# Kernel tuning notes

Measured on AMD Instinct MI355X. Metric: run time of the kernel, lower is better.

## Reference

```python
import jax, jax.numpy as jnp
import numpy as np

V = 50000
E = 800000
B, FIN, FOUT, K = 2, 64, 64, 4


def setup_inputs() -> dict:
    key = jax.random.key(0)
    k1, k2, k3, k4, k5, k6 = jax.random.split(key, 6)
    inputs = jax.random.normal(k1, (B, V, FIN), dtype=jnp.float32)
    weight = jax.random.normal(k2, (K, FIN, FOUT), dtype=jnp.float32) * np.sqrt(2.0 / (FIN * K)).astype(np.float32)
    bias = jax.random.normal(k3, (FOUT,), dtype=jnp.float32)
    lap_vals = jax.random.normal(k4, (E,), dtype=jnp.float32)
    lap_rows = jax.random.randint(k5, (E,), 0, V, dtype=jnp.int32)
    lap_cols = jax.random.randint(k6, (E,), 0, V, dtype=jnp.int32)
    return {"inputs": inputs, "weight": weight, "bias": bias,
            "lap_vals": lap_vals, "lap_rows": lap_rows, "lap_cols": lap_cols}


def reference(inputs, weight, bias, lap_vals, lap_rows, lap_cols):
    B_, V_, Fin = inputs.shape
    K_, _, Fout = weight.shape

    def spmm(x):  # L @ x, L in COO; x: [V, Fin*B]
        return jax.ops.segment_sum(lap_vals[:, None] * x[lap_cols], lap_rows, num_segments=V_)

    # x0: [V, Fin*B] (Fin-major flatten, matching torch permute(1,2,0).view)
    x0 = jnp.transpose(inputs, (1, 2, 0)).reshape(V_, Fin * B_)
    xs = [x0]
    if K_ > 1:
        x1 = spmm(x0)
        xs.append(x1)
        for _ in range(2, K_):
            x2 = 2.0 * spmm(x1) - x0
            xs.append(x2)
            x0, x1 = x1, x2
    # [K,V,Fin,B] -> [B,V,Fin,K] -> [B*V, Fin*K]
    X = jnp.stack(xs).reshape(K_, V_, Fin, B_)
    X = jnp.transpose(X, (3, 1, 2, 0)).reshape(B_ * V_, Fin * K_)
    # faithful to original: weight flattened as (K*Fin, Fout)
    out = X @ weight.reshape(K_ * Fin, Fout)
    return out.reshape(B_, V_, Fout) + bias
```

## Files before the change

kernel.cpp:

```cpp
#include <hip/hip_runtime.h>
#include <hip/hip_bf16.h>


#define NV 50000
#define NE 800000
#define XROW 128
#define NROWS 100000
#define NTILES 6250
#define EPMAX 1600000
#define BSHIFT 7
#define RPB 128
#define NB 391
#define CAP 3072
#define CHUNK 4096
#define P1_BLOCKS 196

using u16 = unsigned short;
using u32 = unsigned int;
using u64 = unsigned long long;
typedef __bf16 bf16x8 __attribute__((ext_vector_type(8)));
typedef float f32x4 __attribute__((ext_vector_type(4)));

__device__ __forceinline__ float bflo(u32 g) { return __uint_as_float(g << 16); }
__device__ __forceinline__ float bfhi(u32 g) { return __uint_as_float(g & 0xffff0000u); }
__device__ __forceinline__ u32 pack_bf2(float a, float b) {
    u16 ha = __builtin_bit_cast(u16, (__bf16)a);
    u16 hb = __builtin_bit_cast(u16, (__bf16)b);
    return (u32)ha | ((u32)hb << 16);
}
__device__ __forceinline__ float unpack_f16hi(u32 rec) {
    u16 h = (u16)(rec >> 16);
    return (float)__builtin_bit_cast(_Float16, h);
}
__device__ __forceinline__ int pad16(int n) { return (n + 15) & ~15; }

__global__ __launch_bounds__(256) void bin1_k(const int* __restrict__ rows, const int* __restrict__ cols,
                                              const float* __restrict__ vals,
                                              int* __restrict__ binctr, u64* __restrict__ tmp) {
    __shared__ int bcnt[NB];
    __shared__ int bofs[NB];
    __shared__ int bcur[NB];
    __shared__ int gbase[NB];
    __shared__ int ps[256];
    __shared__ u64 stage[CHUNK];
    int t = threadIdx.x;
    int base = blockIdx.x * CHUNK;
    int n = NE - base;
    if (n > CHUNK) n = CHUNK;
    if (n <= 0) return;

    for (int i = t; i < NB; i += 256) bcnt[i] = 0;
    __syncthreads();

    for (int i = t; i < n; i += 256) {
        atomicAdd(&bcnt[rows[base + i] >> BSHIFT], 1);
    }
    __syncthreads();

    int i0 = 2 * t, i1 = 2 * t + 1;
    int a0 = (i0 < NB) ? bcnt[i0] : 0;
    int a1 = (i1 < NB) ? bcnt[i1] : 0;
    ps[t] = a0 + a1;
    __syncthreads();
    for (int off = 1; off < 256; off <<= 1) {
        int v = (t >= off) ? ps[t - off] : 0;
        __syncthreads();
        ps[t] += v;
        __syncthreads();
    }
    int eb = ps[t] - (a0 + a1);
    if (i0 < NB) { bofs[i0] = eb;      bcur[i0] = eb;      gbase[i0] = i0 * CAP + atomicAdd(&binctr[i0], a0); }
    if (i1 < NB) { bofs[i1] = eb + a0; bcur[i1] = eb + a0; gbase[i1] = i1 * CAP + atomicAdd(&binctr[i1], a1); }
    __syncthreads();

    for (int i = t; i < n; i += 256) {
        int r = rows[base + i];
        int c = cols[base + i];
        u16 hv = __builtin_bit_cast(u16, (_Float16)vals[base + i]);
        u64 rec = ((u64)(u32)r << 32) | (u64)((u32)c | ((u32)hv << 16));
        int s = atomicAdd(&bcur[r >> BSHIFT], 1);
        stage[s] = rec;
    }
    __syncthreads();

    for (int i = t; i < n; i += 256) {
        u64 rec = stage[i];
        int b = (int)(rec >> (32 + BSHIFT));
        tmp[(size_t)(gbase[b] + (i - bofs[b]))] = rec;
    }
}

__global__ __launch_bounds__(256) void bcnt_k(const u64* __restrict__ tmp, const int* __restrict__ binctr,
                                              int* __restrict__ rowc, int* __restrict__ btot) {
    __shared__ int rc[RPB];
    __shared__ int rs[RPB];
    int b = blockIdx.x, t = threadIdx.x;
    int n = binctr[b];
    const u64* rec = tmp + (size_t)b * CAP;
    if (t < RPB) rc[t] = 0;
    __syncthreads();
    for (int i = t; i < n; i += 256) {
        atomicAdd(&rc[(int)(rec[i] >> 32) & (RPB - 1)], 1);
    }
    __syncthreads();
    if (t < RPB) {
        rowc[b * RPB + t] = rc[t];
        rs[t] = pad16(rc[t]);
    }
    __syncthreads();
    for (int off = 64; off > 0; off >>= 1) {
        if (t < off) rs[t] += rs[t + off];
        __syncthreads();
    }
    if (t == 0) btot[b] = rs[0];
}

__global__ __launch_bounds__(256) void scanb_k(const int* __restrict__ btot, int* __restrict__ bbase,
                                               int* __restrict__ row_ptr) {
    __shared__ int ps[256];
    int t = threadIdx.x;
    int i0 = 2 * t, i1 = 2 * t + 1;
    int a0 = (i0 < NB) ? btot[i0] : 0;
    int a1 = (i1 < NB) ? btot[i1] : 0;
    ps[t] = a0 + a1;
    __syncthreads();
    for (int off = 1; off < 256; off <<= 1) {
        int v = (t >= off) ? ps[t - off] : 0;
        __syncthreads();
        ps[t] += v;
        __syncthreads();
    }
    int eb = ps[t] - (a0 + a1);
    if (i0 < NB) bbase[i0] = eb;
    if (i1 < NB) bbase[i1] = eb + a0;
    if (t == 255) row_ptr[NV] = ps[255];
}

__global__ __launch_bounds__(256) void place_k(const u64* __restrict__ tmp, const int* __restrict__ binctr,
                                               const int* __restrict__ rowc, const int* __restrict__ bbase,
                                               int* __restrict__ row_ptr, u32* __restrict__ epack) {
    __shared__ int rc[RPB];
    __shared__ int ro[RPB];
    int b = blockIdx.x, t = threadIdx.x;
    int n = binctr[b];
    int base = bbase[b];
    const u64* rec = tmp + (size_t)b * CAP;

    int cv = (t < RPB) ? rowc[b * RPB + t] : 0;
    int pv = pad16(cv);
    if (t < RPB) ro[t] = pv;
    __syncthreads();
    for (int off = 1; off < RPB; off <<= 1) {
        int v = 0;
        if (t < RPB && t >= off) v = ro[t - off];
        __syncthreads();
        if (t < RPB) ro[t] += v;
        __syncthreads();
    }
    if (t < RPB) {
        int ex = ro[t] - pv;
        ro[t] = ex;
        rc[t] = 0;
        int v = (b << BSHIFT) + t;
        if (v < NV) row_ptr[v] = base + ex;
    }
    __syncthreads();
    for (int i = t; i < n; i += 256) {
        u64 r64 = rec[i];
        int r = (int)(r64 >> 32) & (RPB - 1);
        int p = base + ro[r] + atomicAdd(&rc[r], 1);
        epack[p] = (u32)r64;
    }
}

__global__ void build_x0_k(const float* __restrict__ in, u32* __restrict__ x0u) {
    int i = blockIdx.x * blockDim.x + threadIdx.x;
    if (i < NV * 64) {
        int v = i >> 6, p = i & 63;
        int b = p >> 5;
        int f = (p & 31) * 2;
        const float* src = in + (size_t)b * (NV * 64) + (size_t)v * 64 + f;
        float2 t = *(const float2*)src;
        x0u[i] = pack_bf2(t.x, t.y);
    }
}

__global__ void prep_w_k(const float* __restrict__ weight, u16* __restrict__ wimg) {
    int i = blockIdx.x * blockDim.x + threadIdx.x;
    if (i < 256 * 64) {
        int c = i >> 6, o = i & 63;
        int cp = ((c & 3) << 6) | (c >> 2);
        wimg[o * 264 + cp] = __builtin_bit_cast(u16, (__bf16)weight[i]);
    }
}

__global__ __launch_bounds__(256) void spmm_k(const u32* __restrict__ x,
                                              const u32* __restrict__ xprev,
                                              const int* __restrict__ row_ptr,
                                              const u32* __restrict__ epack,
                                              u32* __restrict__ xout, int mode) {
    int wave = (int)((blockIdx.x * blockDim.x + threadIdx.x) >> 6);
    u32 lane = threadIdx.x & 63;
    int row = __builtin_amdgcn_readfirstlane(wave);
    if (row >= NV) return;
    int beg = row_ptr[row];
    int end = row_ptr[row + 1];
    int q = (int)(lane >> 4);
    u32 g16 = lane & 15;

    float ax[4] = {0.f, 0.f, 0.f, 0.f};
    float ay[4] = {0.f, 0.f, 0.f, 0.f};

    for (int e = beg; e < end; e += 16) {
        u32 rec[4];
        uint4 gv[4];
        #pragma unroll
        for (int u = 0; u < 4; ++u) {
            rec[u] = epack[e + 4 * u + q];
            gv[u] = *(const uint4*)(x + ((rec[u] & 0xffffu) << 6) + (g16 << 2));
        }
        #pragma unroll
        for (int u = 0; u < 4; ++u) {
            float w = unpack_f16hi(rec[u]);
            ax[0] += w * bflo(gv[u].x); ay[0] += w * bfhi(gv[u].x);
            ax[1] += w * bflo(gv[u].y); ay[1] += w * bfhi(gv[u].y);
            ax[2] += w * bflo(gv[u].z); ay[2] += w * bfhi(gv[u].z);
            ax[3] += w * bflo(gv[u].w); ay[3] += w * bfhi(gv[u].w);
        }
    }

    #pragma unroll
    for (int m = 16; m <= 32; m <<= 1) {
        #pragma unroll
        for (int j = 0; j < 4; ++j) {
            ax[j] += __shfl_xor(ax[j], m, 64);
            ay[j] += __shfl_xor(ay[j], m, 64);
        }
    }

    if (q == 0) {
        if (mode) {
            uint4 pv = *(const uint4*)(xprev + ((u32)row << 6) + (g16 << 2));
            ax[0] = 2.f * ax[0] - bflo(pv.x); ay[0] = 2.f * ay[0] - bfhi(pv.x);
            ax[1] = 2.f * ax[1] - bflo(pv.y); ay[1] = 2.f * ay[1] - bfhi(pv.y);
            ax[2] = 2.f * ax[2] - bflo(pv.z); ay[2] = 2.f * ay[2] - bfhi(pv.z);
            ax[3] = 2.f * ax[3] - bflo(pv.w); ay[3] = 2.f * ay[3] - bfhi(pv.w);
        }
        uint4 o;
        o.x = pack_bf2(ax[0], ay[0]);
        o.y = pack_bf2(ax[1], ay[1]);
        o.z = pack_bf2(ax[2], ay[2]);
        o.w = pack_bf2(ax[3], ay[3]);
        *(uint4*)(xout + ((u32)row << 6) + (g16 << 2)) = o;
    }
}

__global__ __launch_bounds__(256) void final_k(const u16* __restrict__ x_all,
                                               const u16* __restrict__ wimg,
                                               const float* __restrict__ bias,
                                               float* __restrict__ out) {
    __shared__ u16 Wt[64 * 264];
    {
        const u32* src = (const u32*)wimg;
        u32* dst = (u32*)Wt;
        #pragma unroll 4
        for (int i = threadIdx.x; i < 64 * 264 / 2; i += 256) dst[i] = src[i];
    }
    __syncthreads();

    int lane = threadIdx.x & 63;
    int wid = threadIdx.x >> 6;
    int pair = blockIdx.x * 4 + wid;
    int t0 = pair * 2;
    if (t0 >= NTILES) return;

    int m = lane & 15;
    int q8 = (lane >> 4) * 8;

    int r0 = t0 * 16 + m;
    int r1 = r0 + 16;
    const u16* arow0 = x_all + (size_t)(r0 >> 1) * XROW + (r0 & 1) * 64;
    const u16* arow1 = x_all + (size_t)(r1 >> 1) * XROW + (r1 & 1) * 64;

    f32x4 accA[4] = {{0,0,0,0},{0,0,0,0},{0,0,0,0},{0,0,0,0}};
    f32x4 accB[4] = {{0,0,0,0},{0,0,0,0},{0,0,0,0},{0,0,0,0}};

    #pragma unroll
    for (int kb = 0; kb < 8; ++kb) {
        int cb = kb * 32 + q8;
        int arr = cb >> 6;
        int f0 = cb & 63;
        size_t aoff = (size_t)arr * (NV * XROW) + f0;
        bf16x8 a0 = *(const bf16x8*)(arow0 + aoff);
        bf16x8 a1 = *(const bf16x8*)(arow1 + aoff);
        #pragma unroll
        for (int j = 0; j < 4; ++j) {
            bf16x8 bj = *(const bf16x8*)&Wt[(j * 16 + m) * 264 + kb * 32 + q8];
            accA[j] = __builtin_amdgcn_mfma_f32_16x16x32_bf16(a0, bj, accA[j], 0, 0, 0);
            accB[j] = __builtin_amdgcn_mfma_f32_16x16x32_bf16(a1, bj, accB[j], 0, 0, 0);
        }
    }

    float bv[4];
    #pragma unroll
    for (int j = 0; j < 4; ++j) bv[j] = bias[j * 16 + m];

    #pragma unroll
    for (int half = 0; half < 2; ++half) {
        int rbase = (t0 + half) * 16 + (lane >> 4) * 4;
        f32x4* acc = half ? accB : accA;
        #pragma unroll
        for (int reg = 0; reg < 4; ++reg) {
            int rr = rbase + reg;
            float* op = out + (size_t)(rr & 1) * (NV * 64) + (size_t)(rr >> 1) * 64;
            #pragma unroll
            for (int j = 0; j < 4; ++j) op[j * 16 + m] = acc[j][reg] + bv[j];
        }
    }
}

extern "C" void kernel_launch(void* const* d_in, const int* in_sizes, int n_in,
                              void* d_out, int out_size, void* d_ws, size_t ws_size,
                              hipStream_t stream) {
    const float* inputs = (const float*)d_in[0];
    const float* weight = (const float*)d_in[1];
    const float* bias   = (const float*)d_in[2];
    const float* lapv   = (const float*)d_in[3];
    const int*   lrows  = (const int*)d_in[4];
    const int*   lcols  = (const int*)d_in[5];
    float* out = (float*)d_out;

    char* ws = (char*)d_ws;
    size_t o = 0;
    auto alloc = [&](size_t bytes) -> void* {
        void* p = ws + o;
        o += (bytes + 255) & ~(size_t)255;
        return p;
    };
    u16* x_all = (u16*)alloc((size_t)4 * NV * XROW * 2);
    u32* epack = (u32*)alloc((size_t)EPMAX * 4);
    u64* tmp   = (u64*)alloc((size_t)NB * CAP * 8);
    int* row_ptr = (int*)alloc((size_t)(NV + 1) * 4);
    int* binctr  = (int*)alloc((size_t)NB * 4);
    int* btot    = (int*)alloc((size_t)NB * 4);
    int* bbase   = (int*)alloc((size_t)NB * 4);
    int* rowc    = (int*)alloc((size_t)NB * RPB * 4);
    u16* wimg = (u16*)alloc((size_t)64 * 264 * 2);
    (void)ws_size; (void)in_sizes; (void)n_in; (void)out_size;

    u32* x0 = (u32*)(x_all + (size_t)0 * NV * XROW);
    u32* x1 = (u32*)(x_all + (size_t)1 * NV * XROW);
    u32* x2 = (u32*)(x_all + (size_t)2 * NV * XROW);
    u32* x3 = (u32*)(x_all + (size_t)3 * NV * XROW);

    hipMemsetAsync(binctr, 0, (size_t)NB * 4, stream);
    hipMemsetAsync(epack, 0, (size_t)EPMAX * 4, stream);
    bin1_k<<<P1_BLOCKS, 256, 0, stream>>>(lrows, lcols, lapv, binctr, tmp);
    bcnt_k<<<NB, 256, 0, stream>>>(tmp, binctr, rowc, btot);
    scanb_k<<<1, 256, 0, stream>>>(btot, bbase, row_ptr);
    place_k<<<NB, 256, 0, stream>>>(tmp, binctr, rowc, bbase, row_ptr, epack);
    build_x0_k<<<(NV * 64 + 255) / 256, 256, 0, stream>>>(inputs, x0);
    prep_w_k<<<64, 256, 0, stream>>>(weight, wimg);

    spmm_k<<<(NV + 3) / 4, 256, 0, stream>>>(x0, nullptr, row_ptr, epack, x1, 0);
    spmm_k<<<(NV + 3) / 4, 256, 0, stream>>>(x1, x0, row_ptr, epack, x2, 1);
    spmm_k<<<(NV + 3) / 4, 256, 0, stream>>>(x2, x1, row_ptr, epack, x3, 1);

    final_k<<<(NTILES / 2 + 3) / 4, 256, 0, stream>>>(x_all, wimg, bias, out);
}
```

Before: 230.9 us.

## Process two rows per wave in SpMM and zero only padding slots

Each SpMM wave now handles two adjacent rows, interleaving their edge-record and gather loads so more independent memory requests are in flight per wave. The grid shrinks by half. The full memset of the edge array is replaced by zeroing only the padded tail slots of each row inside the placement kernel. This raises register use and adds branch divergence when the two rows have different lengths.

Measured after the change: 239.9 us. +3.9%, slower.

```diff
diff --git a/kernel.cpp b/kernel.cpp
--- a/kernel.cpp
+++ b/kernel.cpp
@@ -14,6 +14,7 @@
 #define CAP 3072
 #define CHUNK 4096
 #define P1_BLOCKS 196
+#define NPAIR 25000
 
 using u16 = unsigned short;
 using u32 = unsigned int;
@@ -171,6 +172,12 @@
         int p = base + ro[r] + atomicAdd(&rc[r], 1);
         epack[p] = (u32)r64;
     }
+    __syncthreads();
+    if (t < RPB) {
+        int s = base + ro[t] + cv;
+        int e = base + ro[t] + pv;
+        for (int i = s; i < e; ++i) epack[i] = 0;
+    }
 }
 
 __global__ void build_x0_k(const float* __restrict__ in, u32* __restrict__ x0u) {
@@ -201,56 +208,95 @@
                                               u32* __restrict__ xout, int mode) {
     int wave = (int)((blockIdx.x * blockDim.x + threadIdx.x) >> 6);
     u32 lane = threadIdx.x & 63;
-    int row = __builtin_amdgcn_readfirstlane(wave);
-    if (row >= NV) return;
-    int beg = row_ptr[row];
-    int end = row_ptr[row + 1];
+    int row0 = __builtin_amdgcn_readfirstlane(wave) * 2;
+    if (row0 >= NV) return;
     int q = (int)(lane >> 4);
     u32 g16 = lane & 15;
 
-    float ax[4] = {0.f, 0.f, 0.f, 0.f};
-    float ay[4] = {0.f, 0.f, 0.f, 0.f};
-
-    for (int e = beg; e < end; e += 16) {
-        u32 rec[4];
-        uint4 gv[4];
-        #pragma unroll
-        for (int u = 0; u < 4; ++u) {
-            rec[u] = epack[e + 4 * u + q];
-            gv[u] = *(const uint4*)(x + ((rec[u] & 0xffffu) << 6) + (g16 << 2));
-        }
-        #pragma unroll
-        for (int u = 0; u < 4; ++u) {
-            float w = unpack_f16hi(rec[u]);
-            ax[0] += w * bflo(gv[u].x); ay[0] += w * bfhi(gv[u].x);
-            ax[1] += w * bflo(gv[u].y); ay[1] += w * bfhi(gv[u].y);
-            ax[2] += w * bflo(gv[u].z); ay[2] += w * bfhi(gv[u].z);
-            ax[3] += w * bflo(gv[u].w); ay[3] += w * bfhi(gv[u].w);
-        }
+    int beg0 = row_ptr[row0];
+    int mid  = row_ptr[row0 + 1];
+    int end1 = row_ptr[row0 + 2];
+
+    float ax0[4] = {0.f,0.f,0.f,0.f}, ay0[4] = {0.f,0.f,0.f,0.f};
+    float ax1[4] = {0.f,0.f,0.f,0.f}, ay1[4] = {0.f,0.f,0.f,0.f};
+
+    int e0 = beg0, e1 = mid;
+    while (e0 < mid || e1 < end1) {
+        bool a0 = e0 < mid, a1 = e1 < end1;
+        u32 rec0[4], rec1[4];
+        uint4 gv0[4], gv1[4];
+        if (a0) {
+            #pragma unroll
+            for (int u = 0; u < 4; ++u) rec0[u] = epack[e0 + 4 * u + q];
+        }
+        if (a1) {
+            #pragma unroll
+            for (int u = 0; u < 4; ++u) rec1[u] = epack[e1 + 4 * u + q];
+        }
+        if (a0) {
+            #pragma unroll
+            for (int u = 0; u < 4; ++u)
+                gv0[u] = *(const uint4*)(x + ((rec0[u] & 0xffffu) << 6) + (g16 << 2));
+        }
+        if (a1) {
+            #pragma unroll
+            for (int u = 0; u < 4; ++u)
+                gv1[u] = *(const uint4*)(x + ((rec1[u] & 0xffffu) << 6) + (g16 << 2));
+        }
+        if (a0) {
+            #pragma unroll
+            for (int u = 0; u < 4; ++u) {
+                float w = unpack_f16hi(rec0[u]);
+                ax0[0] += w * bflo(gv0[u].x); ay0[0] += w * bfhi(gv0[u].x);
+                ax0[1] += w * bflo(gv0[u].y); ay0[1] += w * bfhi(gv0[u].y);
+                ax0[2] += w * bflo(gv0[u].z); ay0[2] += w * bfhi(gv0[u].z);
+                ax0[3] += w * bflo(gv0[u].w); ay0[3] += w * bfhi(gv0[u].w);
+            }
+        }
+        if (a1) {
+            #pragma unroll
+            for (int u = 0; u < 4; ++u) {
+                float w = unpack_f16hi(rec1[u]);
+                ax1[0] += w * bflo(gv1[u].x); ay1[0] += w * bfhi(gv1[u].x);
+                ax1[1] += w * bflo(gv1[u].y); ay1[1] += w * bfhi(gv1[u].y);
+                ax1[2] += w * bflo(gv1[u].z); ay1[2] += w * bfhi(gv1[u].z);
+                ax1[3] += w * bflo(gv1[u].w); ay1[3] += w * bfhi(gv1[u].w);
+            }
+        }
+        e0 += 16; e1 += 16;
     }
 
     #pragma unroll
     for (int m = 16; m <= 32; m <<= 1) {
         #pragma unroll
         for (int j = 0; j < 4; ++j) {
-            ax[j] += __shfl_xor(ax[j], m, 64);
-            ay[j] += __shfl_xor(ay[j], m, 64);
-        }
-    }
-
-    if (q == 0) {
+            ax0[j] += __shfl_xor(ax0[j], m, 64);
+            ay0[j] += __shfl_xor(ay0[j], m, 64);
+            ax1[j] += __shfl_xor(ax1[j], m, 64);
+            ay1[j] += __shfl_xor(ay1[j], m, 64);
+        }
+    }
+
+    if (q < 2) {
+        int row = row0 + q;
+        float bx[4], by[4];
+        #pragma unroll
+        for (int j = 0; j < 4; ++j) {
+            bx[j] = q ? ax1[j] : ax0[j];
+            by[j] = q ? ay1[j] : ay0[j];
+        }
         if (mode) {
             uint4 pv = *(const uint4*)(xprev + ((u32)row << 6) + (g16 << 2));
-            ax[0] = 2.f * ax[0] - bflo(pv.x); ay[0] = 2.f * ay[0] - bfhi(pv.x);
-            ax[1] = 2.f * ax[1] - bflo(pv.y); ay[1] = 2.f * ay[1] - bfhi(pv.y);
-            ax[2] = 2.f * ax[2] - bflo(pv.z); ay[2] = 2.f * ay[2] - bfhi(pv.z);
-            ax[3] = 2.f * ax[3] - bflo(pv.w); ay[3] = 2.f * ay[3] - bfhi(pv.w);
+            bx[0] = 2.f * bx[0] - bflo(pv.x); by[0] = 2.f * by[0] - bfhi(pv.x);
+            bx[1] = 2.f * bx[1] - bflo(pv.y); by[1] = 2.f * by[1] - bfhi(pv.y);
+            bx[2] = 2.f * bx[2] - bflo(pv.z); by[2] = 2.f * by[2] - bfhi(pv.z);
+            bx[3] = 2.f * bx[3] - bflo(pv.w); by[3] = 2.f * by[3] - bfhi(pv.w);
         }
         uint4 o;
-        o.x = pack_bf2(ax[0], ay[0]);
-        o.y = pack_bf2(ax[1], ay[1]);
-        o.z = pack_bf2(ax[2], ay[2]);
-        o.w = pack_bf2(ax[3], ay[3]);
+        o.x = pack_bf2(bx[0], by[0]);
+        o.y = pack_bf2(bx[1], by[1]);
+        o.z = pack_bf2(bx[2], by[2]);
+        o.w = pack_bf2(bx[3], by[3]);
         *(uint4*)(xout + ((u32)row << 6) + (g16 << 2)) = o;
     }
 }
@@ -354,7 +400,6 @@
     u32* x3 = (u32*)(x_all + (size_t)3 * NV * XROW);
 
     hipMemsetAsync(binctr, 0, (size_t)NB * 4, stream);
-    hipMemsetAsync(epack, 0, (size_t)EPMAX * 4, stream);
     bin1_k<<<P1_BLOCKS, 256, 0, stream>>>(lrows, lcols, lapv, binctr, tmp);
     bcnt_k<<<NB, 256, 0, stream>>>(tmp, binctr, rowc, btot);
     scanb_k<<<1, 256, 0, stream>>>(btot, bbase, row_ptr);
@@ -362,9 +407,9 @@
     build_x0_k<<<(NV * 64 + 255) / 256, 256, 0, stream>>>(inputs, x0);
     prep_w_k<<<64, 256, 0, stream>>>(weight, wimg);
 
-    spmm_k<<<(NV + 3) / 4, 256, 0, stream>>>(x0, nullptr, row_ptr, epack, x1, 0);
-    spmm_k<<<(NV + 3) / 4, 256, 0, stream>>>(x1, x0, row_ptr, epack, x2, 1);
-    spmm_k<<<(NV + 3) / 4, 256, 0, stream>>>(x2, x1, row_ptr, epack, x3, 1);
+    spmm_k<<<(NPAIR + 3) / 4, 256, 0, stream>>>(x0, nullptr, row_ptr, epack, x1, 0);
+    spmm_k<<<(NPAIR + 3) / 4, 256, 0, stream>>>(x1, x0, row_ptr, epack, x2, 1);
+    spmm_k<<<(NPAIR + 3) / 4, 256, 0, stream>>>(x2, x1, row_ptr, epack, x3, 1);
 
     final_k<<<(NTILES / 2 + 3) / 4, 256, 0, stream>>>(x_all, wimg, bias, out);
 }
```

## Fuse scan into count kernel, merge prep kernels, pad rows to 32, unroll SpMM 8x

Applied to the files above, without the earlier changes.

Merges the single-block bin scan into the count kernel using a last-block-done atomic ticket, and combines the x0 build and weight prep into one launch. This removes several kernel launches and the large epack memset, which is replaced by zeroing only the padding slots in place_k. Row padding goes from 16 to 32 and the SpMM loop now issues 8 gathers per iteration for more memory-level parallelism. The cost is more padding work on short rows and a threadfence/atomic handshake between blocks.

New measurement: 234.8 us. About the same (+1.7%).

```diff
diff --git a/kernel.cpp b/kernel.cpp
--- a/kernel.cpp
+++ b/kernel.cpp
@@ -7,13 +7,14 @@
 #define XROW 128
 #define NROWS 100000
 #define NTILES 6250
-#define EPMAX 1600000
+#define EPMAX 1700000
 #define BSHIFT 7
 #define RPB 128
 #define NB 391
 #define CAP 3072
 #define CHUNK 4096
 #define P1_BLOCKS 196
+#define X0_BLOCKS 12500
 
 using u16 = unsigned short;
 using u32 = unsigned int;
@@ -32,7 +33,7 @@
     u16 h = (u16)(rec >> 16);
     return (float)__builtin_bit_cast(_Float16, h);
 }
-__device__ __forceinline__ int pad16(int n) { return (n + 15) & ~15; }
+__device__ __forceinline__ int pad32(int n) { return (n + 31) & ~31; }
 
 __global__ __launch_bounds__(256) void bin1_k(const int* __restrict__ rows, const int* __restrict__ cols,
                                               const float* __restrict__ vals,
@@ -91,9 +92,13 @@
 }
 
 __global__ __launch_bounds__(256) void bcnt_k(const u64* __restrict__ tmp, const int* __restrict__ binctr,
-                                              int* __restrict__ rowc, int* __restrict__ btot) {
+                                              int* __restrict__ rowc, int* __restrict__ btot,
+                                              int* __restrict__ done,
+                                              int* __restrict__ bbase, int* __restrict__ row_ptr) {
     __shared__ int rc[RPB];
     __shared__ int rs[RPB];
+    __shared__ int ps[256];
+    __shared__ int flag;
     int b = blockIdx.x, t = threadIdx.x;
     int n = binctr[b];
     const u64* rec = tmp + (size_t)b * CAP;
@@ -105,35 +110,38 @@
     __syncthreads();
     if (t < RPB) {
         rowc[b * RPB + t] = rc[t];
-        rs[t] = pad16(rc[t]);
+        rs[t] = pad32(rc[t]);
     }
     __syncthreads();
     for (int off = 64; off > 0; off >>= 1) {
         if (t < off) rs[t] += rs[t + off];
         __syncthreads();
     }
-    if (t == 0) btot[b] = rs[0];
-}
-
-__global__ __launch_bounds__(256) void scanb_k(const int* __restrict__ btot, int* __restrict__ bbase,
-                                               int* __restrict__ row_ptr) {
-    __shared__ int ps[256];
-    int t = threadIdx.x;
-    int i0 = 2 * t, i1 = 2 * t + 1;
-    int a0 = (i0 < NB) ? btot[i0] : 0;
-    int a1 = (i1 < NB) ? btot[i1] : 0;
-    ps[t] = a0 + a1;
-    __syncthreads();
-    for (int off = 1; off < 256; off <<= 1) {
-        int v = (t >= off) ? ps[t - off] : 0;
-        __syncthreads();
-        ps[t] += v;
-        __syncthreads();
-    }
-    int eb = ps[t] - (a0 + a1);
-    if (i0 < NB) bbase[i0] = eb;
-    if (i1 < NB) bbase[i1] = eb + a0;
-    if (t == 255) row_ptr[NV] = ps[255];
+    if (t == 0) {
+        btot[b] = rs[0];
+        __threadfence();
+        int ticket = atomicAdd(done, 1);
+        flag = (ticket == NB - 1);
+    }
+    __syncthreads();
+    if (flag) {
+        __threadfence();
+        int i0 = 2 * t, i1 = 2 * t + 1;
+        int a0 = (i0 < NB) ? atomicAdd(&btot[i0], 0) : 0;
+        int a1 = (i1 < NB) ? atomicAdd(&btot[i1], 0) : 0;
+        ps[t] = a0 + a1;
+        __syncthreads();
+        for (int off = 1; off < 256; off <<= 1) {
+            int v = (t >= off) ? ps[t - off] : 0;
+            __syncthreads();
+            ps[t] += v;
+            __syncthreads();
+        }
+        int eb = ps[t] - (a0 + a1);
+        if (i0 < NB) bbase[i0] = eb;
+        if (i1 < NB) bbase[i1] = eb + a0;
+        if (t == 255) row_ptr[NV] = ps[255];
+    }
 }
 
 __global__ __launch_bounds__(256) void place_k(const u64* __restrict__ tmp, const int* __restrict__ binctr,
@@ -147,7 +155,7 @@
     const u64* rec = tmp + (size_t)b * CAP;
 
     int cv = (t < RPB) ? rowc[b * RPB + t] : 0;
-    int pv = pad16(cv);
+    int pv = pad32(cv);
     if (t < RPB) ro[t] = pv;
     __syncthreads();
     for (int off = 1; off < RPB; off <<= 1) {
@@ -171,23 +179,27 @@
         int p = base + ro[r] + atomicAdd(&rc[r], 1);
         epack[p] = (u32)r64;
     }
-}
-
-__global__ void build_x0_k(const float* __restrict__ in, u32* __restrict__ x0u) {
-    int i = blockIdx.x * blockDim.x + threadIdx.x;
-    if (i < NV * 64) {
+    __syncthreads();
+    if (t < RPB) {
+        int s = base + ro[t] + cv;
+        int e = base + ro[t] + pv;
+        for (int i = s; i < e; ++i) epack[i] = 0;
+    }
+}
+
+__global__ void bx0w_k(const float* __restrict__ in, u32* __restrict__ x0u,
+                       const float* __restrict__ weight, u16* __restrict__ wimg) {
+    int bid = blockIdx.x;
+    if (bid < X0_BLOCKS) {
+        int i = bid * 256 + threadIdx.x;
         int v = i >> 6, p = i & 63;
         int b = p >> 5;
         int f = (p & 31) * 2;
         const float* src = in + (size_t)b * (NV * 64) + (size_t)v * 64 + f;
         float2 t = *(const float2*)src;
         x0u[i] = pack_bf2(t.x, t.y);
-    }
-}
-
-__global__ void prep_w_k(const float* __restrict__ weight, u16* __restrict__ wimg) {
-    int i = blockIdx.x * blockDim.x + threadIdx.x;
-    if (i < 256 * 64) {
+    } else {
+        int i = (bid - X0_BLOCKS) * 256 + threadIdx.x;
         int c = i >> 6, o = i & 63;
         int cp = ((c & 3) << 6) | (c >> 2);
         wimg[o * 264 + cp] = __builtin_bit_cast(u16, (__bf16)weight[i]);
@@ -211,16 +223,16 @@
     float ax[4] = {0.f, 0.f, 0.f, 0.f};
     float ay[4] = {0.f, 0.f, 0.f, 0.f};
 
-    for (int e = beg; e < end; e += 16) {
-        u32 rec[4];
-        uint4 gv[4];
-        #pragma unroll
-        for (int u = 0; u < 4; ++u) {
-            rec[u] = epack[e + 4 * u + q];
+    for (int e = beg; e < end; e += 32) {
+        u32 rec[8];
+        #pragma unroll
+        for (int u = 0; u < 8; ++u) rec[u] = epack[e + 4 * u + q];
+        uint4 gv[8];
+        #pragma unroll
+        for (int u = 0; u < 8; ++u)
             gv[u] = *(const uint4*)(x + ((rec[u] & 0xffffu) << 6) + (g16 << 2));
-        }
-        #pragma unroll
-        for (int u = 0; u < 4; ++u) {
+        #pragma unroll
+        for (int u = 0; u < 8; ++u) {
             float w = unpack_f16hi(rec[u]);
             ax[0] += w * bflo(gv[u].x); ay[0] += w * bfhi(gv[u].x);
             ax[1] += w * bflo(gv[u].y); ay[1] += w * bfhi(gv[u].y);
@@ -341,26 +353,25 @@
     u32* epack = (u32*)alloc((size_t)EPMAX * 4);
     u64* tmp   = (u64*)alloc((size_t)NB * CAP * 8);
     int* row_ptr = (int*)alloc((size_t)(NV + 1) * 4);
-    int* binctr  = (int*)alloc((size_t)NB * 4);
+    int* binctr  = (int*)alloc((size_t)(NB + 1) * 4);
     int* btot    = (int*)alloc((size_t)NB * 4);
     int* bbase   = (int*)alloc((size_t)NB * 4);
     int* rowc    = (int*)alloc((size_t)NB * RPB * 4);
     u16* wimg = (u16*)alloc((size_t)64 * 264 * 2);
     (void)ws_size; (void)in_sizes; (void)n_in; (void)out_size;
 
+    int* done = binctr + NB;
+
     u32* x0 = (u32*)(x_all + (size_t)0 * NV * XROW);
     u32* x1 = (u32*)(x_all + (size_t)1 * NV * XROW);
     u32* x2 = (u32*)(x_all + (size_t)2 * NV * XROW);
     u32* x3 = (u32*)(x_all + (size_t)3 * NV * XROW);
 
-    hipMemsetAsync(binctr, 0, (size_t)NB * 4, stream);
-    hipMemsetAsync(epack, 0, (size_t)EPMAX * 4, stream);
+    hipMemsetAsync(binctr, 0, (size_t)(NB + 1) * 4, stream);
     bin1_k<<<P1_BLOCKS, 256, 0, stream>>>(lrows, lcols, lapv, binctr, tmp);
-    bcnt_k<<<NB, 256, 0, stream>>>(tmp, binctr, rowc, btot);
-    scanb_k<<<1, 256, 0, stream>>>(btot, bbase, row_ptr);
+    bcnt_k<<<NB, 256, 0, stream>>>(tmp, binctr, rowc, btot, done, bbase, row_ptr);
     place_k<<<NB, 256, 0, stream>>>(tmp, binctr, rowc, bbase, row_ptr, epack);
-    build_x0_k<<<(NV * 64 + 255) / 256, 256, 0, stream>>>(inputs, x0);
-    prep_w_k<<<64, 256, 0, stream>>>(weight, wimg);
+    bx0w_k<<<X0_BLOCKS + 64, 256, 0, stream>>>(inputs, x0, weight, wimg);
 
     spmm_k<<<(NV + 3) / 4, 256, 0, stream>>>(x0, nullptr, row_ptr, epack, x1, 0);
     spmm_k<<<(NV + 3) / 4, 256, 0, stream>>>(x1, x0, row_ptr, epack, x2, 1);
```
